# Kernel optimization log

Hardware: AMD Instinct MI355X
Metric: run time of the kernel (lower is better)

## Reference

```python
import jax, jax.numpy as jnp
import numpy as np

N_BINS = 64
INPUT_DIM = 8
R = 1.2
BOUND = 10.0
BETA = 1e-06
N = 2097152


def _mesh_and_elmt():
    m = N_BINS / 2
    idx = jnp.arange(N_BINS + 1, dtype=jnp.float32) - m
    x1L = BOUND * (R - 1.0) / (R ** m - 1.0)
    xr = (1.0 - R ** jnp.abs(idx)) / (1.0 - R)
    xr = jnp.where(idx >= 0, x1L * xr, -x1L * xr)
    xr = (xr + BOUND) / (2.0 * BOUND)
    mesh = jnp.concatenate([jnp.zeros((1,), jnp.float32), xr[1:-1], jnp.ones((1,), jnp.float32)])  # [n_bins+1]
    elmt = mesh[1:] - mesh[:-1]  # [n_bins]
    return mesh, elmt


def _pdf_normalize(p, elmt):
    # pdf: [n_bins+1, d]; F_ref: [n_bins, d] cumulative bin integrals
    p0 = jnp.full((1, INPUT_DIM), BETA, jnp.float32)
    ep = jnp.exp(p)
    px = ep * ((elmt[:-1] + elmt[1:]) / 2.0)[:, None]
    scale = (1.0 - (elmt[0] + elmt[-1]) * BETA / 2.0) / jnp.sum(px, 0, keepdims=True)
    px = scale * ep
    pdf = jnp.concatenate([p0, px, p0], 0)
    cell = (pdf[:-1] + pdf[1:]) / 2.0 * elmt[:, None]  # [n_bins, d]
    F_ref = jnp.concatenate([jnp.zeros((1, INPUT_DIM), jnp.float32),
                             jnp.cumsum(cell, 0)[:N_BINS - 1]], 0)
    return pdf, F_ref


def setup_inputs() -> dict:
    key = jax.random.key(0)
    k1, k2 = jax.random.split(key)
    x = jax.random.normal(k1, (N, INPUT_DIM), dtype=jnp.float32)
    logdet = jnp.zeros((N, 1), dtype=jnp.float32)
    p = jax.random.normal(k2, (N_BINS - 1, INPUT_DIM), dtype=jnp.float32)
    return {"x": x, "logdet": logdet, "p": p}


def reference(x, logdet, p):
    mesh, elmt = _mesh_and_elmt()
    pdf, F_ref = _pdf_normalize(p, elmt)

    xs = (x + BOUND) / (2.0 * BOUND)  # [N, d] in [0,1] for covered points
    k = jnp.searchsorted(mesh, xs, side='right') - 1  # [N, d]
    cover = (k >= 0) & (k <= N_BINS - 1)
    k = jnp.clip(k, 0, N_BINS - 1)
    col = jnp.arange(INPUT_DIM)[None, :]

    v1 = pdf[k, col]            # [N, d]
    v2 = pdf[k + 1, col]
    xm = xs - mesh[k]
    h = elmt[k]
    F_pre = F_ref[k, col]

    y = jnp.where(cover, F_pre + xm * xm / 2.0 * (v2 - v1) / h + xm * v1, xs)
    dld = jnp.where(cover, xm * (v2 - v1) / h + v1, 1.0)
    logdet = logdet + jnp.sum(jnp.log(dld), -1, keepdims=True)

    y = y * 2.0 * BOUND - BOUND
    y = jnp.where(y > BOUND, BETA * (y - BOUND) + BOUND, y)
    logdet = logdet + jnp.sum(jnp.log(jnp.where(y > BOUND, BETA, 1.0)), -1, keepdims=True)
    y = jnp.where(y < -BOUND, BETA * (y + BOUND) - BOUND, y)
    logdet = logdet + jnp.sum(jnp.log(jnp.where(y < -BOUND, BETA, 1.0)), -1, keepdims=True)
    return y, logdet
```

## Files before the change

### kernel.cpp

```cpp
#include <hip/hip_runtime.h>
#include <hip/hip_bf16.h>
#include <math.h>

#define NPTS   2097152
#define NDIM   8
#define NBINS  64
#define TBL_OFF 80
#define LOG_BETA (-13.815510557964274f)

__global__ void cdfq_prep(const float* __restrict__ p, float* __restrict__ ws) {
    __shared__ float mesh[65];
    __shared__ float elmt[64];
    __shared__ float pdf[65][NDIM];
    __shared__ float Fr[64][NDIM];
    const int t = threadIdx.x;

    if (t < 65) {
        float fidx = (float)t - 32.0f;
        float a = fabsf(fidx);
        float x1L = 10.0f * (1.2f - 1.0f) / (powf(1.2f, 32.0f) - 1.0f);
        float xr = (1.0f - powf(1.2f, a)) / (1.0f - 1.2f);
        xr = (fidx >= 0.0f) ? (x1L * xr) : -(x1L * xr);
        xr = (xr + 10.0f) / 20.0f;
        if (t == 0)  xr = 0.0f;
        if (t == 64) xr = 1.0f;
        mesh[t] = xr;
    }
    __syncthreads();
    if (t < 64) elmt[t] = mesh[t + 1] - mesh[t];
    __syncthreads();

    if (t < NDIM) {
        const int d = t;
        float s = 0.0f;
        for (int i = 0; i < 63; ++i)
            s += expf(p[i * NDIM + d]) * (0.5f * (elmt[i] + elmt[i + 1]));
        float scale = (1.0f - (elmt[0] + elmt[63]) * 1e-6f * 0.5f) / s;
        pdf[0][d]  = 1e-6f;
        pdf[64][d] = 1e-6f;
        for (int i = 0; i < 63; ++i) pdf[i + 1][d] = scale * expf(p[i * NDIM + d]);
        float acc = 0.0f;
        for (int k = 0; k < 64; ++k) {
            Fr[k][d] = acc;
            acc += 0.5f * (pdf[k][d] + pdf[k + 1][d]) * elmt[k];
        }
    }
    __syncthreads();

    if (t < 65) ws[t] = mesh[t];
    float4* tbl = (float4*)(ws + TBL_OFF);
    for (int idx = t; idx < NDIM * NBINS; idx += blockDim.x) {
        int d = idx >> 6, k = idx & 63;
        float v1 = pdf[k][d];
        float v2 = pdf[k + 1][d];
        tbl[idx] = make_float4(v1, (v2 - v1) / elmt[k], Fr[k][d], mesh[k]);
    }
}

__global__ __launch_bounds__(256) void cdfq_main(const float* __restrict__ x,
                                                 const float* __restrict__ logdet_in,
                                                 const float* __restrict__ ws,
                                                 float* __restrict__ y_out,
                                                 float* __restrict__ ld_out,
                                                 int n) {
    __shared__ float  smesh[65];
    __shared__ float4 stbl[NDIM * NBINS];

    const int t = threadIdx.x;
    for (int i = t; i < 65; i += 256) smesh[i] = ws[i];
    const float4* wt = (const float4*)(ws + TBL_OFF);
    for (int i = t; i < NDIM * NBINS; i += 256) stbl[i] = wt[i];
    __syncthreads();

    const int stride = gridDim.x * blockDim.x;
    for (int i = blockIdx.x * blockDim.x + t; i < n; i += stride) {
        const float4* xv = (const float4*)x + 2 * (size_t)i;
        float4 xa = xv[0];
        float4 xb = xv[1];
        float ld = logdet_in[i];

        float xd[8] = {xa.x, xa.y, xa.z, xa.w, xb.x, xb.y, xb.z, xb.w};
        float yd[8];
        float lsum = 0.0f;

#pragma unroll
        for (int d = 0; d < 8; ++d) {
            float xs = (xd[d] + 10.0f) / 20.0f;
            int k = 0;
            if (xs >= smesh[32])     k = 32;
            if (xs >= smesh[k + 16]) k += 16;
            if (xs >= smesh[k + 8])  k += 8;
            if (xs >= smesh[k + 4])  k += 4;
            if (xs >= smesh[k + 2])  k += 2;
            if (xs >= smesh[k + 1])  k += 1;

            float4 tb = stbl[(d << 6) + k];
            float xm  = xs - tb.w;
            bool cov  = (xs >= 0.0f) && (xs < 1.0f);

            float ycov = tb.z + xm * xm * 0.5f * tb.y + xm * tb.x;
            float dld  = cov ? (xm * tb.y + tb.x) : 1.0f;
            float yy   = cov ? ycov : xs;

            lsum += logf(dld);

            yy = yy * 20.0f - 10.0f;
            if (yy > 10.0f)  { yy = 1e-6f * (yy - 10.0f) + 10.0f; lsum += LOG_BETA; }
            if (yy < -10.0f) { yy = 1e-6f * (yy + 10.0f) - 10.0f; lsum += LOG_BETA; }
            yd[d] = yy;
        }

        float4* yo = (float4*)y_out + 2 * (size_t)i;
        yo[0] = make_float4(yd[0], yd[1], yd[2], yd[3]);
        yo[1] = make_float4(yd[4], yd[5], yd[6], yd[7]);
        ld_out[i] = ld + lsum;
    }
}

extern "C" void kernel_launch(void* const* d_in, const int* in_sizes, int n_in,
                              void* d_out, int out_size, void* d_ws, size_t ws_size,
                              hipStream_t stream) {
    const float* x      = (const float*)d_in[0];
    const float* logdet = (const float*)d_in[1];
    const float* p      = (const float*)d_in[2];
    float* ws = (float*)d_ws;

    const int n = in_sizes[1];
    float* y_out  = (float*)d_out;
    float* ld_out = (float*)d_out + (size_t)n * NDIM;

    cdfq_prep<<<1, 256, 0, stream>>>(p, ws);

    const int block = 256;
    const int grid  = 2048;
    cdfq_main<<<grid, block, 0, stream>>>(x, logdet, ws, y_out, ld_out, n);
}
```

Baseline: 154.7 us.

## Fuse table prep into main kernel and compute bin index analytically

Drops the separate single-block prep kernel. Every block now rebuilds the normalized pdf and CDF table in shared memory, using wave shuffles for the sum and the prefix scan. The binary search over the geometric mesh is replaced by a closed-form log2-based bin index. The per-dimension logf calls become pairwise-product __log2f calls. This removes one launch and the serialized prep latency, and cuts per-element ALU and LDS work, at the cost of redundant per-block table setup and possible off-by-one binning or underflow/precision risk near bin edges.

Result: faster. 140.1 us (-9.4%).

```diff
diff --git a/kernel.cpp b/kernel.cpp
--- a/kernel.cpp
+++ b/kernel.cpp
@@ -2,74 +2,82 @@
 #include <hip/hip_bf16.h>
 #include <math.h>
 
-#define NPTS   2097152
 #define NDIM   8
 #define NBINS  64
-#define TBL_OFF 80
-#define LOG_BETA (-13.815510557964274f)
+#define LOG_BETA   (-13.815510557964274f)
+#define LN2F       0.69314718055994531f
+#define ALPHA      34.0821892f
+#define INV_LOG2R  3.80178401692393f
 
-__global__ void cdfq_prep(const float* __restrict__ p, float* __restrict__ ws) {
-    __shared__ float mesh[65];
-    __shared__ float elmt[64];
-    __shared__ float pdf[65][NDIM];
-    __shared__ float Fr[64][NDIM];
+__global__ __launch_bounds__(256) void cdfq_fused(const float* __restrict__ x,
+                                                  const float* __restrict__ logdet_in,
+                                                  const float* __restrict__ p,
+                                                  float* __restrict__ y_out,
+                                                  float* __restrict__ ld_out,
+                                                  int n)
+{
+    __shared__ float  mesh[65];
+    __shared__ float  elmt[64];
+    __shared__ float  sc[NDIM];
+    __shared__ float  pdfs[NDIM][65];
+    __shared__ float  cell[NDIM][64];
+    __shared__ float4 stbl[NDIM * NBINS];
+
     const int t = threadIdx.x;
 
     if (t < 65) {
         float fidx = (float)t - 32.0f;
         float a = fabsf(fidx);
-        float x1L = 10.0f * (1.2f - 1.0f) / (powf(1.2f, 32.0f) - 1.0f);
-        float xr = (1.0f - powf(1.2f, a)) / (1.0f - 1.2f);
-        xr = (fidx >= 0.0f) ? (x1L * xr) : -(x1L * xr);
+        float x1L = 2.0f / (powf(1.2f, 32.0f) - 1.0f);
+        float xr = x1L * (powf(1.2f, a) - 1.0f) / 0.2f;
+        xr = (fidx >= 0.0f) ? xr : -xr;
         xr = (xr + 10.0f) / 20.0f;
         if (t == 0)  xr = 0.0f;
         if (t == 64) xr = 1.0f;
         mesh[t] = xr;
     }
+    for (int idx = t; idx < 63 * NDIM; idx += 256) {
+        int d = idx & 7, k = idx >> 3;
+        pdfs[d][k + 1] = expf(p[k * NDIM + d]);
+    }
+    if (t < NDIM) { pdfs[t][0] = 1e-6f; pdfs[t][64] = 1e-6f; }
     __syncthreads();
     if (t < 64) elmt[t] = mesh[t + 1] - mesh[t];
     __syncthreads();
 
-    if (t < NDIM) {
-        const int d = t;
-        float s = 0.0f;
-        for (int i = 0; i < 63; ++i)
-            s += expf(p[i * NDIM + d]) * (0.5f * (elmt[i] + elmt[i + 1]));
-        float scale = (1.0f - (elmt[0] + elmt[63]) * 1e-6f * 0.5f) / s;
-        pdf[0][d]  = 1e-6f;
-        pdf[64][d] = 1e-6f;
-        for (int i = 0; i < 63; ++i) pdf[i + 1][d] = scale * expf(p[i * NDIM + d]);
-        float acc = 0.0f;
-        for (int k = 0; k < 64; ++k) {
-            Fr[k][d] = acc;
-            acc += 0.5f * (pdf[k][d] + pdf[k + 1][d]) * elmt[k];
+    if (t < 64) {
+        for (int d = 0; d < NDIM; ++d) {
+            float w = 0.0f;
+            if (t < 63) w = pdfs[d][t + 1] * 0.5f * (elmt[t] + elmt[t + 1]);
+            for (int off = 32; off > 0; off >>= 1) w += __shfl_down(w, off);
+            if (t == 0) sc[d] = (1.0f - (elmt[0] + elmt[63]) * 5e-7f) / w;
         }
     }
     __syncthreads();
-
-    if (t < 65) ws[t] = mesh[t];
-    float4* tbl = (float4*)(ws + TBL_OFF);
-    for (int idx = t; idx < NDIM * NBINS; idx += blockDim.x) {
+    for (int idx = t; idx < 63 * NDIM; idx += 256) {
+        int d = idx & 7, k = idx >> 3;
+        pdfs[d][k + 1] *= sc[d];
+    }
+    __syncthreads();
+    for (int idx = t; idx < NDIM * NBINS; idx += 256) {
         int d = idx >> 6, k = idx & 63;
-        float v1 = pdf[k][d];
-        float v2 = pdf[k + 1][d];
-        tbl[idx] = make_float4(v1, (v2 - v1) / elmt[k], Fr[k][d], mesh[k]);
+        cell[d][k] = 0.5f * (pdfs[d][k] + pdfs[d][k + 1]) * elmt[k];
     }
-}
-
-__global__ __launch_bounds__(256) void cdfq_main(const float* __restrict__ x,
-                                                 const float* __restrict__ logdet_in,
-                                                 const float* __restrict__ ws,
-                                                 float* __restrict__ y_out,
-                                                 float* __restrict__ ld_out,
-                                                 int n) {
-    __shared__ float  smesh[65];
-    __shared__ float4 stbl[NDIM * NBINS];
-
-    const int t = threadIdx.x;
-    for (int i = t; i < 65; i += 256) smesh[i] = ws[i];
-    const float4* wt = (const float4*)(ws + TBL_OFF);
-    for (int i = t; i < NDIM * NBINS; i += 256) stbl[i] = wt[i];
+    __syncthreads();
+    if (t < 64) {
+        for (int d = 0; d < NDIM; ++d) {
+            float c0 = cell[d][t];
+            float v = c0;
+            for (int off = 1; off < 64; off <<= 1) {
+                float w = __shfl_up(v, off);
+                if (t >= off) v += w;
+            }
+            float Fpre = v - c0;
+            float v1 = pdfs[d][t];
+            float v2 = pdfs[d][t + 1];
+            stbl[d * 64 + t] = make_float4(v1, (v2 - v1) / elmt[t], Fpre, mesh[t]);
+        }
+    }
     __syncthreads();
 
     const int stride = gridDim.x * blockDim.x;
@@ -80,40 +88,43 @@
         float ld = logdet_in[i];
 
         float xd[8] = {xa.x, xa.y, xa.z, xa.w, xb.x, xb.y, xb.z, xb.w};
-        float yd[8];
-        float lsum = 0.0f;
+        float yd[8], dd[8];
 
 #pragma unroll
         for (int d = 0; d < 8; ++d) {
-            float xs = (xd[d] + 10.0f) / 20.0f;
-            int k = 0;
-            if (xs >= smesh[32])     k = 32;
-            if (xs >= smesh[k + 16]) k += 16;
-            if (xs >= smesh[k + 8])  k += 8;
-            if (xs >= smesh[k + 4])  k += 4;
-            if (xs >= smesh[k + 2])  k += 2;
-            if (xs >= smesh[k + 1])  k += 1;
+            float xo = xd[d];
+            float xs = fmaf(xo, 0.05f, 0.5f);
+            float u  = fabsf(xo);
+            float g  = __log2f(fmaf(ALPHA, u, 1.0f)) * INV_LOG2R;
+            int jp = (int)fminf(g, 31.0f);
+            int jn = (int)ceilf(fminf(g, 32.0f));
+            int k  = (xo >= 0.0f) ? (32 + jp) : (32 - jn);
 
             float4 tb = stbl[(d << 6) + k];
             float xm  = xs - tb.w;
             bool cov  = (xs >= 0.0f) && (xs < 1.0f);
 
-            float ycov = tb.z + xm * xm * 0.5f * tb.y + xm * tb.x;
-            float dld  = cov ? (xm * tb.y + tb.x) : 1.0f;
-            float yy   = cov ? ycov : xs;
+            float yc = tb.z + xm * fmaf(0.5f * xm, tb.y, tb.x);
+            float dl = fmaf(xm, tb.y, tb.x);
+            float yy = cov ? yc : xs;
+            dd[d]    = cov ? dl : 1.0f;
 
-            lsum += logf(dld);
-
-            yy = yy * 20.0f - 10.0f;
-            if (yy > 10.0f)  { yy = 1e-6f * (yy - 10.0f) + 10.0f; lsum += LOG_BETA; }
-            if (yy < -10.0f) { yy = 1e-6f * (yy + 10.0f) - 10.0f; lsum += LOG_BETA; }
+            yy = fmaf(yy, 20.0f, -10.0f);
+            if (yy > 10.0f)  { yy = fmaf(1e-6f, yy - 10.0f, 10.0f);  ld += LOG_BETA; }
+            if (yy < -10.0f) { yy = fmaf(1e-6f, yy + 10.0f, -10.0f); ld += LOG_BETA; }
             yd[d] = yy;
         }
+
+        float l01 = __log2f(dd[0] * dd[1]);
+        float l23 = __log2f(dd[2] * dd[3]);
+        float l45 = __log2f(dd[4] * dd[5]);
+        float l67 = __log2f(dd[6] * dd[7]);
+        ld = fmaf((l01 + l23) + (l45 + l67), LN2F, ld);
 
         float4* yo = (float4*)y_out + 2 * (size_t)i;
         yo[0] = make_float4(yd[0], yd[1], yd[2], yd[3]);
         yo[1] = make_float4(yd[4], yd[5], yd[6], yd[7]);
-        ld_out[i] = ld + lsum;
+        ld_out[i] = ld;
     }
 }
 
@@ -123,15 +134,12 @@
     const float* x      = (const float*)d_in[0];
     const float* logdet = (const float*)d_in[1];
     const float* p      = (const float*)d_in[2];
-    float* ws = (float*)d_ws;
 
     const int n = in_sizes[1];
     float* y_out  = (float*)d_out;
     float* ld_out = (float*)d_out + (size_t)n * NDIM;
 
-    cdfq_prep<<<1, 256, 0, stream>>>(p, ws);
-
     const int block = 256;
     const int grid  = 2048;
-    cdfq_main<<<grid, block, 0, stream>>>(x, logdet, ws, y_out, ld_out, n);
+    cdfq_fused<<<grid, block, 0, stream>>>(x, logdet, p, y_out, ld_out, n);
 }
```
